# Kernel tuning notes

Hardware: AMD Instinct MI355X
Metric: run time of the kernel (lower is better)

## Reference

```python
import jax, jax.numpy as jnp
import numpy as np
from jax.scipy.special import digamma

N, D, K = 32768, 64, 64


def setup_inputs() -> dict:
    key = jax.random.key(0)
    k1, k2, k3, k4, k5, k6, k7 = jax.random.split(key, 7)
    X = jax.random.normal(k1, (N, D), dtype=jnp.float32)
    means = jax.random.normal(k2, (K, D), dtype=jnp.float32)
    # Upper-triangular precision Cholesky factors with strictly positive diagonal
    # (matches solve_triangular(L, I).T from the torch code).
    off = jnp.triu(jax.random.normal(k3, (K, D, D), dtype=jnp.float32) * 0.05, 1)
    diag = jnp.exp(jax.random.normal(k4, (K, D), dtype=jnp.float32) * 0.1)
    precisions_chol = off + jax.vmap(jnp.diag)(diag)
    weight_concentration = jax.random.uniform(k5, (2, K), dtype=jnp.float32, minval=0.5, maxval=5.0)
    # degrees_of_freedom must be > D - 1 so digamma args stay positive
    degrees_of_freedom = jnp.float32(D) + jax.random.uniform(k6, (K,), dtype=jnp.float32, minval=1.0, maxval=50.0)
    mean_precision = jax.random.uniform(k7, (K,), dtype=jnp.float32, minval=0.5, maxval=10.0)
    return {"X": X, "means": means, "precisions_chol": precisions_chol,
            "weight_concentration": weight_concentration,
            "degrees_of_freedom": degrees_of_freedom, "mean_precision": mean_precision}


def _weighted_log_prob(X, means, precisions_chol, weight_concentration,
                       degrees_of_freedom, mean_precision):
    n_features = X.shape[1]
    # log|prec_chol_k| = sum of log of diagonal entries
    log_det = jnp.sum(jnp.log(jnp.diagonal(precisions_chol, axis1=1, axis2=2)), axis=1)  # [K]
    # whitened residuals: y[n,k,:] = X[n] @ P_k - mu_k @ P_k
    XP = jnp.einsum('nd,kde->nke', X, precisions_chol)            # [N,K,D]
    muP = jnp.einsum('kd,kde->ke', means, precisions_chol)        # [K,D]
    sq = jnp.sum(jnp.square(XP - muP[None]), axis=-1)             # [N,K]
    log2pi = jnp.log(jnp.float32(2.0 * np.pi))
    log_gauss = -0.5 * (n_features * log2pi + sq) + log_det[None]
    # Bayesian corrections
    log_gauss = log_gauss - 0.5 * n_features * jnp.log(degrees_of_freedom)[None]
    i = jnp.arange(n_features, dtype=jnp.float32)
    log_lambda = n_features * jnp.log(jnp.float32(2.0)) + jnp.sum(
        digamma(0.5 * (degrees_of_freedom[None, :] - i[:, None])), axis=0)  # [K]
    log_prob = log_gauss + 0.5 * (log_lambda - n_features / mean_precision)[None]
    # stick-breaking log weights (dirichlet_process)
    a, b = weight_concentration[0], weight_concentration[1]
    dsum = digamma(a + b)
    log_w = digamma(a) - dsum + jnp.concatenate(
        [jnp.zeros((1,), dtype=X.dtype), jnp.cumsum(digamma(b) - dsum)[:-1]])
    return log_prob + log_w[None]


def reference(X, means, precisions_chol, weight_concentration,
              degrees_of_freedom, mean_precision):
    wlp = _weighted_log_prob(X, means, precisions_chol, weight_concentration,
                             degrees_of_freedom, mean_precision)
    return jnp.argmax(wlp, axis=1)
```

## Files before the change

kernel.cpp:

```cpp
#include <hip/hip_runtime.h>
#include <math.h>

#define N_ROWS 32768
#define DIM 64
#define KCOMP 64
#define KSPLIT 8
#define KLOCAL 8
#define THREADS 256
#define ROWS_PER_BLOCK 128
#define ROWS_PER_WAVE 32

#define PT_K_BYTES 16384

#define LOG2PI_D 1.8378770664093454836

typedef _Float16 f16x8 __attribute__((ext_vector_type(8)));
typedef float f32x4 __attribute__((ext_vector_type(4)));

__device__ __forceinline__ double digamma_d(double x) {
  double r = 0.0;
  while (x < 6.0) { r -= 1.0 / x; x += 1.0; }
  double inv = 1.0 / x;
  double inv2 = inv * inv;
  double s = log(x) - 0.5 * inv
      - inv2 * (1.0/12.0 - inv2 * (1.0/120.0 - inv2 * (1.0/252.0
      - inv2 * (1.0/240.0 - inv2 * (1.0/132.0)))));
  return r + s;
}

__global__ void prep1_kernel(const float* __restrict__ means,
                             const float* __restrict__ P,
                             const float* __restrict__ wc,
                             const float* __restrict__ dof,
                             const float* __restrict__ mp,
                             char*   __restrict__ Pt,
                             float*  __restrict__ muP,
                             double* __restrict__ t_arr,
                             double* __restrict__ g_arr,
                             double* __restrict__ pc_arr)
{
  __shared__ float lds[DIM][DIM + 1];
  const int k = blockIdx.x;
  const int t = threadIdx.x;
  const float* Pk = P + k * DIM * DIM;

  for (int i = t; i < DIM * DIM; i += THREADS)
    lds[i >> 6][i & 63] = Pk[i];
  __syncthreads();

  char* dst = Pt + (size_t)k * PT_K_BYTES;
#pragma unroll
  for (int cc = 0; cc < 4; ++cc) {
    int cid  = cc * THREADS + t;
    int blk  = cid >> 7;
    int sel  = (cid >> 6) & 1;
    int lane = cid & 63;
    int et = blk >> 1, c = blk & 1;
    int m = lane & 15, q = lane >> 4;
    int e = et * 16 + m;
    int d0 = c * 32 + q * 8;
    f16x8 o;
#pragma unroll
    for (int j = 0; j < 8; ++j) {
      float v = lds[d0 + j][e];
      _Float16 h = (_Float16)v;
      o[j] = sel ? (_Float16)(v - (float)h) : h;
    }
    *(f16x8*)(dst + cid * 16) = o;
  }

  if (t < 64) {
    const int i = t;
    const float* mk = means + k * DIM;
    float acc = 0.f;
#pragma unroll 8
    for (int d = 0; d < DIM; ++d) acc = fmaf(mk[d], lds[d][i], acc);
    muP[k * DIM + i] = acc;

    double dofk = (double)dof[k];
    double s1 = digamma_d(0.5 * (dofk - (double)i));
    double s2 = log((double)lds[i][i]);
#pragma unroll
    for (int off = 32; off > 0; off >>= 1) {
      s1 += __shfl_down(s1, off);
      s2 += __shfl_down(s2, off);
    }
    if (i == 0) {
      double ak = (double)wc[k], bk = (double)wc[KCOMP + k];
      double dgab = digamma_d(ak + bk);
      double log_lambda = (double)DIM * log(2.0) + s1;
      double pc = s2
                - 0.5 * (double)DIM * LOG2PI_D
                - 0.5 * (double)DIM * log(dofk)
                + 0.5 * (log_lambda - (double)DIM / (double)mp[k]);
      t_arr[k] = digamma_d(bk) - dgab;
      g_arr[k] = digamma_d(ak) - dgab;
      pc_arr[k] = pc;
    }
  }
}

__global__ __launch_bounds__(THREADS, 4) void main_kernel(
    const float* __restrict__ X,
    const char*  __restrict__ Pt,
    const float* __restrict__ muP,
    const double* __restrict__ t_arr,
    const double* __restrict__ g_arr,
    const double* __restrict__ pc_arr,
    float* __restrict__ pval,
    int*   __restrict__ pidx)
{
  __shared__ float cvec_lds[KCOMP];

  const int tid  = threadIdx.x;
  const int wave = tid >> 6;
  const int lane = tid & 63;
  const int m    = lane & 15;
  const int q    = lane >> 4;
  const int ks   = blockIdx.y;
  const int rowbase = blockIdx.x * ROWS_PER_BLOCK + wave * ROWS_PER_WAVE;

  if (tid < 64) {
    double t = t_arr[tid];
    double s = t;
#pragma unroll
    for (int off = 1; off < 64; off <<= 1) {
      double v = __shfl_up(s, off);
      if (tid >= off) s += v;
    }
    cvec_lds[tid] = (float)(pc_arr[tid] + g_arr[tid] + (s - t));
  }

  f16x8 ahi[2][2], alo[2][2];
#pragma unroll
  for (int rt = 0; rt < 2; ++rt) {
    int row = rowbase + rt * 16 + m;
    const float* xp = X + row * DIM;
#pragma unroll
    for (int c = 0; c < 2; ++c) {
      const float4* xq4 = (const float4*)(xp + c * 32 + q * 8);
      float4 v0 = xq4[0], v1 = xq4[1];
      float xv[8] = {v0.x, v0.y, v0.z, v0.w, v1.x, v1.y, v1.z, v1.w};
      f16x8 h, l;
#pragma unroll
      for (int j = 0; j < 8; ++j) {
        _Float16 hv = (_Float16)xv[j];
        h[j] = hv;
        l[j] = (_Float16)(xv[j] - (float)hv);
      }
      ahi[rt][c] = h;
      alo[rt][c] = l;
    }
  }

  __syncthreads();

  float best = -INFINITY;
  int   bidx = 0;
  const bool b0 = (m & 1), b1 = (m & 2), b2 = (m & 4);

  for (int ki = 0; ki < KLOCAL; ++ki) {
    const int k = ks * KLOCAL + ki;
    const char* pk = Pt + (size_t)k * PT_K_BYTES;
    const float ck = cvec_lds[k];
    float sq[8] = {0.f,0.f,0.f,0.f,0.f,0.f,0.f,0.f};

#pragma unroll
    for (int et = 0; et < 4; ++et) {
      const float mval = -muP[k * DIM + et * 16 + m];
      f32x4 acc[2];
#pragma unroll
      for (int rt = 0; rt < 2; ++rt)
#pragma unroll
        for (int r = 0; r < 4; ++r) acc[rt][r] = mval;

#pragma unroll
      for (int c = 0; c < 2; ++c) {
        const char* bp = pk + ((et * 2 + c) << 11) + (lane << 4);
        f16x8 bh = *(const f16x8*)bp;
        f16x8 bl = *(const f16x8*)(bp + 1024);
#pragma unroll
        for (int rt = 0; rt < 2; ++rt) {
          acc[rt] = __builtin_amdgcn_mfma_f32_16x16x32_f16(ahi[rt][c], bh, acc[rt], 0, 0, 0);
          acc[rt] = __builtin_amdgcn_mfma_f32_16x16x32_f16(ahi[rt][c], bl, acc[rt], 0, 0, 0);
          acc[rt] = __builtin_amdgcn_mfma_f32_16x16x32_f16(alo[rt][c], bh, acc[rt], 0, 0, 0);
        }
      }
#pragma unroll
      for (int rt = 0; rt < 2; ++rt)
#pragma unroll
        for (int r = 0; r < 4; ++r)
          sq[rt * 4 + r] = fmaf(acc[rt][r], acc[rt][r], sq[rt * 4 + r]);
    }

    float w4[4];
#pragma unroll
    for (int p = 0; p < 4; ++p) {
      float keep = b0 ? sq[2*p+1] : sq[2*p];
      float send = b0 ? sq[2*p]   : sq[2*p+1];
      w4[p] = keep + __shfl_xor(send, 1);
    }
    float u2[2];
#pragma unroll
    for (int p = 0; p < 2; ++p) {
      float keep = b1 ? w4[2*p+1] : w4[2*p];
      float send = b1 ? w4[2*p]   : w4[2*p+1];
      u2[p] = keep + __shfl_xor(send, 2);
    }
    float keep = b2 ? u2[1] : u2[0];
    float send = b2 ? u2[0] : u2[1];
    float z = keep + __shfl_xor(send, 4);
    z += __shfl_xor(z, 8);

    float wv = fmaf(-0.5f, z, ck);
    if (wv > best || (wv == best && k < bidx)) { best = wv; bidx = k; }
  }

  if (m < 8) {
    int rt = (m >> 2) & 1, r = m & 3;
    int row = rowbase + rt * 16 + q * 4 + r;
    pval[ks * N_ROWS + row] = best;
    pidx[ks * N_ROWS + row] = bidx;
  }
}

__global__ void reduce_kernel(const float* __restrict__ pval,
                              const int* __restrict__ pidx,
                              int* __restrict__ out)
{
  int n = blockIdx.x * blockDim.x + threadIdx.x;
  if (n >= N_ROWS) return;
  float best = -INFINITY; int bi = 0;
  for (int ks = 0; ks < KSPLIT; ++ks) {
    float v = pval[ks * N_ROWS + n];
    int   i = pidx[ks * N_ROWS + n];
    if (v > best || (v == best && i < bi)) { best = v; bi = i; }
  }
  out[n] = bi;
}

extern "C" void kernel_launch(void* const* d_in, const int* in_sizes, int n_in,
                              void* d_out, int out_size, void* d_ws, size_t ws_size,
                              hipStream_t stream) {
  const float* X     = (const float*)d_in[0];
  const float* means = (const float*)d_in[1];
  const float* P     = (const float*)d_in[2];
  const float* wc    = (const float*)d_in[3];
  const float* dof   = (const float*)d_in[4];
  const float* mp    = (const float*)d_in[5];
  int* out = (int*)d_out;

  char* wsb = (char*)d_ws;
  float*  muP    = (float*)(wsb);
  double* t_arr  = (double*)(wsb + 16640);
  double* g_arr  = (double*)(wsb + 17152);
  double* pc_arr = (double*)(wsb + 17664);
  char*   Pt     = wsb + 32768;
  float*  pval   = (float*)(wsb + 32768 + (size_t)KCOMP * PT_K_BYTES);
  int*    pidx   = (int*)(wsb + 32768 + (size_t)KCOMP * PT_K_BYTES
                          + (size_t)KSPLIT * N_ROWS * sizeof(float));

  prep1_kernel<<<KCOMP, THREADS, 0, stream>>>(means, P, wc, dof, mp, Pt,
                                              muP, t_arr, g_arr, pc_arr);

  dim3 grid(N_ROWS / ROWS_PER_BLOCK, KSPLIT);
  main_kernel<<<grid, THREADS, 0, stream>>>(X, Pt, muP, t_arr, g_arr, pc_arr,
                                            pval, pidx);

  reduce_kernel<<<(N_ROWS + 255) / 256, 256, 0, stream>>>(pval, pidx, out);
}
```

Measured before the change: 125.5 us.

## Fuse split-K argmax reduction into main kernel and prefetch next component's weights

Removes the separate reduce kernel: each row-group block bumps an atomic counter, and the last of the K-split blocks reduces the partial argmax results and writes the output. The main loop also prefetches the first precision tile of the next component into registers while the current one is finishing. The per-split muP slice is staged in LDS instead of read from global memory per iteration. This saves a kernel launch and hides some load latency, at the cost of a memset, atomics and fences, plus extra register pressure under launch bounds of 4.

```diff
diff --git a/kernel.cpp b/kernel.cpp
--- a/kernel.cpp
+++ b/kernel.cpp
@@ -9,6 +9,7 @@
 #define THREADS 256
 #define ROWS_PER_BLOCK 128
 #define ROWS_PER_WAVE 32
+#define ROWGROUPS (N_ROWS / ROWS_PER_BLOCK)
 
 #define PT_K_BYTES 16384
 
@@ -108,9 +109,13 @@
     const double* __restrict__ g_arr,
     const double* __restrict__ pc_arr,
     float* __restrict__ pval,
-    int*   __restrict__ pidx)
+    int*   __restrict__ pidx,
+    int*   __restrict__ cnt,
+    int*   __restrict__ out)
 {
   __shared__ float cvec_lds[KCOMP];
+  __shared__ float mup_lds[KLOCAL * DIM];
+  __shared__ int is_last;
 
   const int tid  = threadIdx.x;
   const int wave = tid >> 6;
@@ -130,6 +135,9 @@
     }
     cvec_lds[tid] = (float)(pc_arr[tid] + g_arr[tid] + (s - t));
   }
+#pragma unroll
+  for (int i = tid; i < KLOCAL * DIM; i += THREADS)
+    mup_lds[i] = muP[ks * KLOCAL * DIM + i];
 
   f16x8 ahi[2][2], alo[2][2];
 #pragma unroll
@@ -159,6 +167,17 @@
   int   bidx = 0;
   const bool b0 = (m & 1), b1 = (m & 2), b2 = (m & 4);
 
+  f16x8 pbh[2], pbl[2];
+  {
+    const char* pk0 = Pt + (size_t)(ks * KLOCAL) * PT_K_BYTES;
+#pragma unroll
+    for (int c = 0; c < 2; ++c) {
+      const char* bp = pk0 + (c << 11) + (lane << 4);
+      pbh[c] = *(const f16x8*)bp;
+      pbl[c] = *(const f16x8*)(bp + 1024);
+    }
+  }
+
   for (int ki = 0; ki < KLOCAL; ++ki) {
     const int k = ks * KLOCAL + ki;
     const char* pk = Pt + (size_t)k * PT_K_BYTES;
@@ -167,7 +186,7 @@
 
 #pragma unroll
     for (int et = 0; et < 4; ++et) {
-      const float mval = -muP[k * DIM + et * 16 + m];
+      const float mval = -mup_lds[(ki << 6) + et * 16 + m];
       f32x4 acc[2];
 #pragma unroll
       for (int rt = 0; rt < 2; ++rt)
@@ -176,9 +195,13 @@
 
 #pragma unroll
       for (int c = 0; c < 2; ++c) {
-        const char* bp = pk + ((et * 2 + c) << 11) + (lane << 4);
-        f16x8 bh = *(const f16x8*)bp;
-        f16x8 bl = *(const f16x8*)(bp + 1024);
+        f16x8 bh, bl;
+        if (et == 0) { bh = pbh[c]; bl = pbl[c]; }
+        else {
+          const char* bp = pk + ((et * 2 + c) << 11) + (lane << 4);
+          bh = *(const f16x8*)bp;
+          bl = *(const f16x8*)(bp + 1024);
+        }
 #pragma unroll
         for (int rt = 0; rt < 2; ++rt) {
           acc[rt] = __builtin_amdgcn_mfma_f32_16x16x32_f16(ahi[rt][c], bh, acc[rt], 0, 0, 0);
@@ -193,6 +216,17 @@
           sq[rt * 4 + r] = fmaf(acc[rt][r], acc[rt][r], sq[rt * 4 + r]);
     }
 
+    {
+      const int kn = (ki + 1 < KLOCAL) ? (k + 1) : k;
+      const char* npk = Pt + (size_t)kn * PT_K_BYTES;
+#pragma unroll
+      for (int c = 0; c < 2; ++c) {
+        const char* bp = npk + (c << 11) + (lane << 4);
+        pbh[c] = *(const f16x8*)bp;
+        pbl[c] = *(const f16x8*)(bp + 1024);
+      }
+    }
+
     float w4[4];
 #pragma unroll
     for (int p = 0; p < 4; ++p) {
@@ -222,21 +256,28 @@
     pval[ks * N_ROWS + row] = best;
     pidx[ks * N_ROWS + row] = bidx;
   }
-}
-
-__global__ void reduce_kernel(const float* __restrict__ pval,
-                              const int* __restrict__ pidx,
-                              int* __restrict__ out)
-{
-  int n = blockIdx.x * blockDim.x + threadIdx.x;
-  if (n >= N_ROWS) return;
-  float best = -INFINITY; int bi = 0;
-  for (int ks = 0; ks < KSPLIT; ++ks) {
-    float v = pval[ks * N_ROWS + n];
-    int   i = pidx[ks * N_ROWS + n];
-    if (v > best || (v == best && i < bi)) { best = v; bi = i; }
-  }
-  out[n] = bi;
+
+  __threadfence();
+  __syncthreads();
+  if (tid == 0) {
+    int old = atomicAdd(&cnt[blockIdx.x], 1);
+    is_last = (old == KSPLIT - 1);
+  }
+  __syncthreads();
+  if (is_last) {
+    __threadfence();
+    if (tid < ROWS_PER_BLOCK) {
+      int n = blockIdx.x * ROWS_PER_BLOCK + tid;
+      float bv = -INFINITY; int bi = 0;
+#pragma unroll
+      for (int s = 0; s < KSPLIT; ++s) {
+        float v = pval[s * N_ROWS + n];
+        int   i = pidx[s * N_ROWS + n];
+        if (v > bv || (v == bv && i < bi)) { bv = v; bi = i; }
+      }
+      out[n] = bi;
+    }
+  }
 }
 
 extern "C" void kernel_launch(void* const* d_in, const int* in_sizes, int n_in,
@@ -255,17 +296,18 @@
   double* t_arr  = (double*)(wsb + 16640);
   double* g_arr  = (double*)(wsb + 17152);
   double* pc_arr = (double*)(wsb + 17664);
+  int*    cnt    = (int*)(wsb + 20480);
   char*   Pt     = wsb + 32768;
   float*  pval   = (float*)(wsb + 32768 + (size_t)KCOMP * PT_K_BYTES);
   int*    pidx   = (int*)(wsb + 32768 + (size_t)KCOMP * PT_K_BYTES
                           + (size_t)KSPLIT * N_ROWS * sizeof(float));
 
+  hipMemsetAsync(cnt, 0, ROWGROUPS * sizeof(int), stream);
+
   prep1_kernel<<<KCOMP, THREADS, 0, stream>>>(means, P, wc, dof, mp, Pt,
                                               muP, t_arr, g_arr, pc_arr);
 
-  dim3 grid(N_ROWS / ROWS_PER_BLOCK, KSPLIT);
+  dim3 grid(ROWGROUPS, KSPLIT);
   main_kernel<<<grid, THREADS, 0, stream>>>(X, Pt, muP, t_arr, g_arr, pc_arr,
-                                            pval, pidx);
-
-  reduce_kernel<<<(N_ROWS + 255) / 256, 256, 0, stream>>>(pval, pidx, out);
+                                            pval, pidx, cnt, out);
 }
```

New measurement: 270.5 us. 115% more time.
